# Kernel optimization log

Measured on AMD Instinct MI355X. Metric: run time of the kernel, lower is better.

The kernel has to match this reference:

```python
import jax, jax.numpy as jnp
import numpy as np

B, S, E, H, L, F = 64, 256, 480, 6, 8, 1920
D = E // H  # 80
VOCAB, MEL, CHORD = 4833, 257, 4833 - 257
EPS = 1e-5


def setup_inputs() -> dict:
    key = jax.random.key(0)
    ks = jax.random.split(key, 24)
    mel = jax.random.randint(ks[0], (B, S), 0, MEL)
    chd = MEL + jax.random.randint(ks[1], (B, S), 0, CHORD)
    pos = jnp.arange(S) % 2  # 0=melody, 1=chord
    input_tokens = jnp.where(pos[None, :] == 1, chd, mel)
    std = 0.02
    n = lambda k, shp: std * jax.random.normal(k, shp, dtype=jnp.float32)
    return {
        'input_tokens': input_tokens,
        'tok_emb': n(ks[2], (VOCAB, E)),
        'pos_emb': n(ks[3], (S, E)),
        'Wq': n(ks[4], (L, E, E)), 'bq': jnp.zeros((L, E)),
        'Wk': n(ks[5], (L, E, E)), 'bk': jnp.zeros((L, E)),
        'Wv': n(ks[6], (L, E, E)), 'bv': jnp.zeros((L, E)),
        'Wo': n(ks[7], (L, E, E)), 'bo': jnp.zeros((L, E)),
        'ln1_s': jnp.ones((L, E)), 'ln1_b': jnp.zeros((L, E)),
        'ln2_s': jnp.ones((L, E)), 'ln2_b': jnp.zeros((L, E)),
        'W1': n(ks[8], (L, F, E)), 'b1': jnp.zeros((L, F)),
        'W2': n(ks[9], (L, E, F)), 'b2': jnp.zeros((L, E)),
        'Wh': n(ks[10], (CHORD, E)), 'bh': jnp.zeros((CHORD,)),
    }


def _ln(x, s, b):
    mu = jnp.mean(x, -1, keepdims=True)
    var = jnp.var(x, -1, keepdims=True)
    return (x - mu) * jax.lax.rsqrt(var + EPS) * s + b


def reference(input_tokens, tok_emb, pos_emb, Wq, bq, Wk, bk, Wv, bv, Wo, bo,
              ln1_s, ln1_b, ln2_s, ln2_b, W1, b1, W2, b2, Wh, bh):
    x = tok_emb[input_tokens] + pos_emb[None, :, :]  # [B,S,E]
    causal = jnp.tril(jnp.ones((S, S), dtype=bool))  # True = keep
    scale = 1.0 / jnp.sqrt(jnp.float32(D))
    for i in range(L):
        h = _ln(x, ln1_s[i], ln1_b[i])
        q = (h @ Wq[i].T + bq[i]).reshape(B, S, H, D).transpose(0, 2, 1, 3)
        k = (h @ Wk[i].T + bk[i]).reshape(B, S, H, D).transpose(0, 2, 1, 3)
        v = (h @ Wv[i].T + bv[i]).reshape(B, S, H, D).transpose(0, 2, 1, 3)
        scores = jnp.einsum('bhsd,bhtd->bhst', q, k) * scale
        scores = jnp.where(causal[None, None], scores, -jnp.inf)
        attn = jax.nn.softmax(scores, axis=-1)
        o = jnp.einsum('bhst,bhtd->bhsd', attn, v)
        o = o.transpose(0, 2, 1, 3).reshape(B, S, E)
        x = x + (o @ Wo[i].T + bo[i])
        h2 = _ln(x, ln2_s[i], ln2_b[i])
        ff = jax.nn.gelu(h2 @ W1[i].T + b1[i], approximate=False) @ W2[i].T + b2[i]
        x = x + ff
    chord = x[:, 1::2, :]  # [B, S//2, E]
    return chord @ Wh.T + bh
```

## Files before the change

kernel.cpp:

```cpp
#include <hip/hip_runtime.h>
#include <hip/hip_bf16.h>
#include <math.h>

#define B_ 64
#define S_ 256
#define E_ 480
#define H_ 6
#define D_ 80
#define L_ 8
#define F_ 1920
#define CHORD_ 4576
#define TOKENS_ (B_*S_)
#define CROWS_ (B_*128)
#define QS_ 1440

typedef unsigned short u16;
typedef unsigned int u32;
typedef unsigned long long u64;
typedef __attribute__((ext_vector_type(8))) short short8;
typedef __attribute__((ext_vector_type(4))) float f32x4;
typedef __attribute__((ext_vector_type(4))) u32 u32x4;

__device__ __forceinline__ u16 f2bf(float f){
  u32 u = __float_as_uint(f);
  return (u16)((u + 0x7fffu + ((u >> 16) & 1u)) >> 16);
}

__device__ __forceinline__ void async_cp16(void* lds, const void* g){
  __builtin_amdgcn_global_load_lds((const __attribute__((address_space(1))) void*)g,
                                   (__attribute__((address_space(3))) void*)lds, 16, 0, 0);
}

__device__ __forceinline__ void xcd_tile(int gx, int gy, int& tx, int& ty){
  const int nwg = gx * gy;
  const int bid = blockIdx.y * gx + blockIdx.x;
  const int xcd = bid & 7, slot = bid >> 3;
  const int q8 = nwg >> 3, r8 = nwg & 7;
  const int t = slot + (xcd < r8 ? xcd * (q8 + 1) : r8 * (q8 + 1) + (xcd - r8) * q8);
  ty = t / gx;
  tx = t - ty * gx;
}

__global__ void cvt_kernel(const float* __restrict__ s, u16* __restrict__ d, int n4)
{
  int i = blockIdx.x * 256 + threadIdx.x;
  const int stride = gridDim.x * 256;
  for (; i < n4; i += stride){
    float4 v = ((const float4*)s)[i];
    u64 w = (u64)((u32)f2bf(v.x) | ((u32)f2bf(v.y) << 16))
          | ((u64)((u32)f2bf(v.z) | ((u32)f2bf(v.w) << 16)) << 32);
    ((u64*)d)[i] = w;
  }
}

__global__ void qkv_cvt_kernel(const float* __restrict__ Wq, const float* __restrict__ Wk,
                               const float* __restrict__ Wv, u16* __restrict__ dst)
{
  const int per = E_*E_/4;
  const int tot = L_*3*per;
  int i = blockIdx.x * 256 + threadIdx.x;
  const int stride = gridDim.x * 256;
  for (; i < tot; i += stride){
    int l = i / (3*per);
    int rem = i - l*3*per;
    int sel = rem / per;
    int r2 = rem - sel*per;
    const float* src = (sel == 0) ? Wq : (sel == 1) ? Wk : Wv;
    float4 v = ((const float4*)(src + (size_t)l*E_*E_))[r2];
    u64 w = (u64)((u32)f2bf(v.x) | ((u32)f2bf(v.y) << 16))
          | ((u64)((u32)f2bf(v.z) | ((u32)f2bf(v.w) << 16)) << 32);
    ((u64*)dst)[i] = w;
  }
}

__global__ void bias_cat_kernel(const float* __restrict__ bq, const float* __restrict__ bk,
                                const float* __restrict__ bv, float* __restrict__ dst)
{
  int i = blockIdx.x * 256 + threadIdx.x;
  if (i >= L_*QS_) return;
  int l = i / QS_, c = i - l*QS_;
  float v = (c < 480) ? bq[l*480 + c] : (c < 960) ? bk[l*480 + c - 480] : bv[l*480 + c - 960];
  dst[i] = v;
}

__global__ void embed_kernel(const int* __restrict__ tok,
                             const float* __restrict__ tok_emb,
                             const float* __restrict__ pos_emb,
                             float* __restrict__ x)
{
  int row = blockIdx.x;
  int s = row & (S_-1);
  int t = tok[row];
  const float* te = tok_emb + (size_t)t * E_;
  const float* pe = pos_emb + (size_t)s * E_;
  float* xr = x + (size_t)row * E_;
  for (int e = threadIdx.x; e < E_; e += blockDim.x)
    xr[e] = te[e] + pe[e];
}

__global__ __launch_bounds__(256) void ln_kernel(const float* __restrict__ x,
    const float* __restrict__ g, const float* __restrict__ b, u16* __restrict__ o)
{
  int wid = threadIdx.x >> 6, lane = threadIdx.x & 63;
  int row = blockIdx.x * 4 + wid;
  const float* xr = x + (size_t)row * E_;
  float v[8];
  #pragma unroll
  for (int i = 0; i < 7; ++i) v[i] = xr[lane + i*64];
  v[7] = (lane < 32) ? xr[448 + lane] : 0.f;
  float sum = 0.f, sq = 0.f;
  #pragma unroll
  for (int i = 0; i < 8; ++i){ sum += v[i]; sq += v[i]*v[i]; }
  #pragma unroll
  for (int m = 1; m < 64; m <<= 1){ sum += __shfl_xor(sum, m); sq += __shfl_xor(sq, m); }
  float mean = sum * (1.f/E_);
  float var  = sq  * (1.f/E_) - mean*mean;
  float rs = rsqrtf(var + 1e-5f);
  u16* orow = o + (size_t)row * E_;
  #pragma unroll
  for (int i = 0; i < 7; ++i){
    int idx = lane + i*64;
    orow[idx] = f2bf((v[i]-mean)*rs*g[idx] + b[idx]);
  }
  if (lane < 32){
    int idx = 448 + lane;
    orow[idx] = f2bf((v[7]-mean)*rs*g[idx] + b[idx]);
  }
}

template<int MODE>
__global__ __launch_bounds__(256, 4) void gemm_bf_kernel(const u16* __restrict__ A,
                            const u16* __restrict__ Wb, const float* __restrict__ bias,
                            u16* __restrict__ Cb, float* __restrict__ Cf,
                            int M, int N, int K, int ldc)
{
  __shared__ u16 As[2][128*32];
  __shared__ u16 Ws[2][128*32];
  const int tid = threadIdx.x;
  const int wid = tid >> 6, lane = tid & 63;
  const int wr = wid >> 1, wc = wid & 1;
  const int lr = lane & 15, kg = lane >> 4;
  const int kgs = kg ^ (lr & 3);
  int tx, ty;
  xcd_tile(gridDim.x, gridDim.y, tx, ty);
  const int m0 = ty * 128;
  const int n0 = tx * 128;

  const f32x4 zero = {0.f,0.f,0.f,0.f};
  f32x4 acc[4][4];
  #pragma unroll
  for (int i=0;i<4;i++)
    #pragma unroll
    for (int j=0;j<4;j++)
      acc[i][j] = zero;

  const int srow = tid >> 2;
  const int schunk = (tid & 3) ^ (srow & 3);
  const u16* ap0 = A + (size_t)(m0 + srow) * K + schunk*8;
  const u16* ap1 = ap0 + (size_t)64 * K;
  int r0 = n0 + srow, r1 = r0 + 64;
  if (r0 >= N) r0 = N-1;
  if (r1 >= N) r1 = N-1;
  const u16* wp0 = Wb + (size_t)r0 * K + schunk*8;
  const u16* wp1 = Wb + (size_t)r1 * K + schunk*8;

  #define STAGE(bb, k0) do { \
    char* ab = (char*)As[bb] + wid*1024; \
    char* wb_ = (char*)Ws[bb] + wid*1024; \
    async_cp16(ab,        ap0 + (k0)); \
    async_cp16(ab + 4096, ap1 + (k0)); \
    async_cp16(wb_,        wp0 + (k0)); \
    async_cp16(wb_ + 4096, wp1 + (k0)); \
  } while(0)

  const int nsteps = K >> 5;
  STAGE(0, 0);
  __syncthreads();
  int cur = 0;
  for (int ks = 0; ks < nsteps; ++ks){
    if (ks + 1 < nsteps) STAGE(cur^1, (ks+1) << 5);

    short8 af[4], wf[4];
    #pragma unroll
    for (int i=0;i<4;i++) af[i] = *(const short8*)&As[cur][(wr*64 + i*16 + lr)*32 + kgs*8];
    #pragma unroll
    for (int j=0;j<4;j++) wf[j] = *(const short8*)&Ws[cur][(wc*64 + j*16 + lr)*32 + kgs*8];
    #pragma unroll
    for (int i=0;i<4;i++)
      #pragma unroll
      for (int j=0;j<4;j++)
        acc[i][j] = __builtin_amdgcn_mfma_f32_16x16x32_bf16(af[i], wf[j], acc[i][j], 0, 0, 0);

    __syncthreads();
    cur ^= 1;
  }
  #undef STAGE

  #pragma unroll
  for (int i=0;i<4;i++){
    const int row = m0 + wr*64 + i*16 + kg*4;
    #pragma unroll
    for (int j=0;j<4;j++){
      const int col = n0 + wc*64 + j*16 + lr;
      if (col < N){
        const float bv = bias[col];
        #pragma unroll
        for (int q=0;q<4;q++){
          float val = acc[i][j][q] + bv;
          size_t off = (size_t)(row + q) * ldc + col;
          if (MODE == 0){
            Cb[off] = f2bf(val);
          } else if (MODE == 1){
            float gx = 0.5f * val * (1.f + erff(val * 0.70710678118654752f));
            Cb[off] = f2bf(gx);
          } else if (MODE == 2){
            Cf[off] += val;
          } else {
            Cf[off] = val;
          }
        }
      }
    }
  }
}

template<int MODE>
__global__ __launch_bounds__(256) void gemm_kernel(const u16* __restrict__ A, const float* __restrict__ W,
                            const float* __restrict__ bias,
                            u16* __restrict__ Cb, float* __restrict__ Cf,
                            int M, int N, int K, int ldc)
{
  __shared__ u16 As[128*32];
  __shared__ u16 Ws[128*32];
  const int tid = threadIdx.x;
  const int wid = tid >> 6, lane = tid & 63;
  const int wr = wid >> 1, wc = wid & 1;
  const int lr = lane & 15, kg = lane >> 4;
  int tx, ty;
  xcd_tile(gridDim.x, gridDim.y, tx, ty);
  const int m0 = ty * 128;
  const int n0 = tx * 128;

  const f32x4 zero = {0.f,0.f,0.f,0.f};
  f32x4 acc[4][4];
  #pragma unroll
  for (int i=0;i<4;i++)
    #pragma unroll
    for (int j=0;j<4;j++)
      acc[i][j] = zero;

  const int trow = tid >> 1;
  const int tcol = (tid & 1) * 16;
  const int wn = n0 + trow;
  const bool wok = wn < N;
  const float* wp = W + (size_t)wn * K + tcol;

  const u16* ap0 = A + (size_t)(m0 + (tid>>2)) * K + (tid&3)*8;
  const u16* ap1 = ap0 + (size_t)64 * K;
  char* lb0 = (char*)As + wid*1024;
  char* lb1 = (char*)As + 4096 + wid*1024;
  u32* wdst = (u32*)&Ws[trow*32 + tcol];

  const int nsteps = K >> 5;
  for (int ks = 0; ks < nsteps; ++ks){
    const int k0 = ks << 5;
    async_cp16(lb0, ap0 + k0);
    async_cp16(lb1, ap1 + k0);

    float wv[16];
    if (wok){
      const float4* s4 = (const float4*)(wp + k0);
      #pragma unroll
      for (int i=0;i<4;i++){
        float4 t4 = s4[i];
        wv[4*i]=t4.x; wv[4*i+1]=t4.y; wv[4*i+2]=t4.z; wv[4*i+3]=t4.w;
      }
    } else {
      #pragma unroll
      for (int i=0;i<16;i++) wv[i]=0.f;
    }
    u32 pk[8];
    #pragma unroll
    for (int i=0;i<8;i++) pk[i] = (u32)f2bf(wv[2*i]) | ((u32)f2bf(wv[2*i+1]) << 16);
    #pragma unroll
    for (int i=0;i<8;i++) wdst[i] = pk[i];

    __syncthreads();

    short8 af[4], wf[4];
    #pragma unroll
    for (int i=0;i<4;i++) af[i] = *(const short8*)&As[(wr*64 + i*16 + lr)*32 + kg*8];
    #pragma unroll
    for (int j=0;j<4;j++) wf[j] = *(const short8*)&Ws[(wc*64 + j*16 + lr)*32 + kg*8];
    #pragma unroll
    for (int i=0;i<4;i++)
      #pragma unroll
      for (int j=0;j<4;j++)
        acc[i][j] = __builtin_amdgcn_mfma_f32_16x16x32_bf16(af[i], wf[j], acc[i][j], 0, 0, 0);

    __syncthreads();
  }

  #pragma unroll
  for (int i=0;i<4;i++){
    const int row = m0 + wr*64 + i*16 + kg*4;
    #pragma unroll
    for (int j=0;j<4;j++){
      const int col = n0 + wc*64 + j*16 + lr;
      if (col < N){
        const float bv = bias[col];
        #pragma unroll
        for (int q=0;q<4;q++){
          float val = acc[i][j][q] + bv;
          size_t off = (size_t)(row + q) * ldc + col;
          if (MODE == 0){
            Cb[off] = f2bf(val);
          } else if (MODE == 1){
            float gx = 0.5f * val * (1.f + erff(val * 0.70710678118654752f));
            Cb[off] = f2bf(gx);
          } else if (MODE == 2){
            Cf[off] += val;
          } else {
            Cf[off] = val;
          }
        }
      }
    }
  }
}

#define KSTRIDE 104
#define VSTRIDE 264
__global__ __launch_bounds__(256) void attn_mfma_kernel(const u16* __restrict__ QKV,
                                                        u16* __restrict__ O)
{
  __shared__ u16 ks[256*KSTRIDE];
  __shared__ u16 vt[80*VSTRIDE];
  const int bh = blockIdx.x;
  const int b = bh / H_, h = bh - b*H_;
  const int tid = threadIdx.x;
  const int wv = tid >> 6, lane = tid & 63;
  const int q16 = lane & 15, g = lane >> 4;
  const size_t rowbase = (size_t)(b*S_ + tid) * QS_ + h * D_;

  {
    const uint4* kr = (const uint4*)(QKV + rowbase + 480);
    uint4 t0[10];
    #pragma unroll
    for (int i=0;i<10;i++) t0[i] = kr[i];
    u16* krow = &ks[tid*KSTRIDE];
    #pragma unroll
    for (int i=0;i<10;i++) *(uint4*)&krow[i*8] = t0[i];
    const uint4 z4 = {0,0,0,0};
    *(uint4*)&krow[80] = z4;
    *(uint4*)&krow[88] = z4;
  }
  {
    const u32* vr = (const u32*)(QKV + rowbase + 960);
    u32 t1[40];
    #pragma unroll
    for (int i=0;i<40;i++) t1[i] = vr[i];
    #pragma unroll
    for (int i=0;i<40;i++){
      vt[(2*i)*VSTRIDE + tid]   = (u16)(t1[i] & 0xffffu);
      vt[(2*i+1)*VSTRIDE + tid] = (u16)(t1[i] >> 16);
    }
  }
  short8 bq[4][3];
  const short8 z8 = {0,0,0,0,0,0,0,0};
  #pragma unroll
  for (int i=0;i<4;i++){
    const int qr = 16*wv + 64*i;
    const u16* qrow = QKV + (size_t)(b*S_ + qr + q16) * QS_ + h*D_;
    bq[i][0] = *(const short8*)&qrow[g*8];
    bq[i][1] = *(const short8*)&qrow[32 + g*8];
    bq[i][2] = (g < 2) ? *(const short8*)&qrow[64 + g*8] : z8;
  }
  __syncthreads();

  f32x4 o_[4][5];
  float m_[4], l_[4];
  #pragma unroll
  for (int i=0;i<4;i++){
    m_[i] = -1e30f; l_[i] = 0.f;
    #pragma unroll
    for (int j=0;j<5;j++) o_[i][j] = (f32x4){0.f,0.f,0.f,0.f};
  }
  const float scale = 0.1118033988749895f;
  const int ktmaxw = (16*wv + 207) >> 5;

  for (int kt = 0; kt <= ktmaxw; ++kt){
    short8 af[2][3];
    #pragma unroll
    for (int a=0;a<2;a++)
      #pragma unroll
      for (int kk=0;kk<3;kk++)
        af[a][kk] = *(const short8*)&ks[(32*kt + 16*a + q16)*KSTRIDE + kk*32 + g*8];
    short8 bvv[5];
    #pragma unroll
    for (int j=0;j<5;j++)
      bvv[j] = *(const short8*)&vt[(16*j + q16)*VSTRIDE + kt*32 + g*8];

    #pragma unroll
    for (int i=0;i<4;i++){
      const int qr = 16*wv + 64*i;
      if (kt > ((qr + 15) >> 5)) continue;
      f32x4 c0 = {0.f,0.f,0.f,0.f}, c1 = {0.f,0.f,0.f,0.f};
      #pragma unroll
      for (int kk=0;kk<3;kk++){
        c0 = __builtin_amdgcn_mfma_f32_16x16x32_bf16(af[0][kk], bq[i][kk], c0, 0, 0, 0);
        c1 = __builtin_amdgcn_mfma_f32_16x16x32_bf16(af[1][kk], bq[i][kk], c1, 0, 0, 0);
      }
      const int qglob = qr + q16;
      const int kb0 = 32*kt + 4*g;
      const bool diag = (32*kt + 31) > qr;
      float s0[4], s1[4];
      #pragma unroll
      for (int r=0;r<4;r++){
        s0[r] = c0[r] * scale;
        s1[r] = c1[r] * scale;
        if (diag){
          if (kb0 + r > qglob)      s0[r] = -3e38f;
          if (kb0 + 16 + r > qglob) s1[r] = -3e38f;
        }
      }
      float mx = fmaxf(fmaxf(fmaxf(s0[0],s0[1]),fmaxf(s0[2],s0[3])),
                       fmaxf(fmaxf(s1[0],s1[1]),fmaxf(s1[2],s1[3])));
      mx = fmaxf(mx, __shfl_xor(mx, 16));
      mx = fmaxf(mx, __shfl_xor(mx, 32));
      const float mnew = fmaxf(m_[i], mx);
      const float resc = __expf(m_[i] - mnew);
      float p0[4], p1[4], ps = 0.f;
      #pragma unroll
      for (int r=0;r<4;r++){
        p0[r] = __expf(s0[r] - mnew);
        p1[r] = __expf(s1[r] - mnew);
        ps += p0[r] + p1[r];
      }
      ps += __shfl_xor(ps, 16);
      ps += __shfl_xor(ps, 32);
      l_[i] = l_[i] * resc + ps;
      m_[i] = mnew;
      float fr[4];
      #pragma unroll
      for (int r=0;r<4;r++) fr[r] = __shfl(resc, 4*g + r);
      #pragma unroll
      for (int j=0;j<5;j++){
        #pragma unroll
        for (int r=0;r<4;r++) o_[i][j][r] *= fr[r];
      }
      u32 pw0 = (u32)f2bf(p0[0]) | ((u32)f2bf(p0[1]) << 16);
      u32 pw1 = (u32)f2bf(p0[2]) | ((u32)f2bf(p0[3]) << 16);
      u32 pw2 = (u32)f2bf(p1[0]) | ((u32)f2bf(p1[1]) << 16);
      u32 pw3 = (u32)f2bf(p1[2]) | ((u32)f2bf(p1[3]) << 16);
      const int s01 = ((((g<<1)&3)<<4) + q16) << 2;
      const int s23 = (((((g<<1)+1)&3)<<4) + q16) << 2;
      int rA0 = __builtin_amdgcn_ds_bpermute(s01, (int)pw0);
      int rB0 = __builtin_amdgcn_ds_bpermute(s01, (int)pw2);
      int rA1 = __builtin_amdgcn_ds_bpermute(s01, (int)pw1);
      int rB1 = __builtin_amdgcn_ds_bpermute(s01, (int)pw3);
      int rA2 = __builtin_amdgcn_ds_bpermute(s23, (int)pw0);
      int rB2 = __builtin_amdgcn_ds_bpermute(s23, (int)pw2);
      int rA3 = __builtin_amdgcn_ds_bpermute(s23, (int)pw1);
      int rB3 = __builtin_amdgcn_ds_bpermute(s23, (int)pw3);
      const bool lo = (g < 2);
      u32x4 rw = { (u32)(lo ? rA0 : rB0), (u32)(lo ? rA1 : rB1),
                   (u32)(lo ? rA2 : rB2), (u32)(lo ? rA3 : rB3) };
      short8 pa = __builtin_bit_cast(short8, rw);
      #pragma unroll
      for (int j=0;j<5;j++)
        o_[i][j] = __builtin_amdgcn_mfma_f32_16x16x32_bf16(pa, bvv[j], o_[i][j], 0, 0, 0);
    }
  }

  #pragma unroll
  for (int i=0;i<4;i++){
    const int qr = 16*wv + 64*i;
    const float inv = 1.f / l_[i];
    float fr[4];
    #pragma unroll
    for (int r=0;r<4;r++) fr[r] = __shfl(inv, 4*g + r);
    #pragma unroll
    for (int j=0;j<5;j++){
      #pragma unroll
      for (int r=0;r<4;r++){
        const int row = qr + 4*g + r;
        O[(size_t)(b*S_ + row) * E_ + h*D_ + 16*j + q16] = f2bf(o_[i][j][r] * fr[r]);
      }
    }
  }
}

__global__ void gather_kernel(const float* __restrict__ x, u16* __restrict__ cin)
{
  int i = blockIdx.x * 256 + threadIdx.x;
  if (i >= CROWS_*E_) return;
  int row = i / E_, col = i - row*E_;
  int b = row >> 7, r = row & 127;
  cin[i] = f2bf(x[((size_t)(b*S_ + 2*r + 1))*E_ + col]);
}

extern "C" void kernel_launch(void* const* d_in, const int* in_sizes, int n_in,
                              void* d_out, int out_size, void* d_ws, size_t ws_size,
                              hipStream_t stream)
{
  (void)in_sizes; (void)n_in; (void)out_size;
  const int*   tok     = (const int*)d_in[0];
  const float* tok_emb = (const float*)d_in[1];
  const float* pos_emb = (const float*)d_in[2];
  const float* Wq = (const float*)d_in[3];
  const float* bq = (const float*)d_in[4];
  const float* Wk = (const float*)d_in[5];
  const float* bk = (const float*)d_in[6];
  const float* Wv = (const float*)d_in[7];
  const float* bv = (const float*)d_in[8];
  const float* Wo = (const float*)d_in[9];
  const float* bo = (const float*)d_in[10];
  const float* ln1s = (const float*)d_in[11];
  const float* ln1b = (const float*)d_in[12];
  const float* ln2s = (const float*)d_in[13];
  const float* ln2b = (const float*)d_in[14];
  const float* W1 = (const float*)d_in[15];
  const float* b1 = (const float*)d_in[16];
  const float* W2 = (const float*)d_in[17];
  const float* b2 = (const float*)d_in[18];
  const float* Wh = (const float*)d_in[19];
  const float* bh = (const float*)d_in[20];

  char* p = (char*)d_ws;
  float* x  = (float*)p;            p += (size_t)TOKENS_*E_*4;
  u16* h    = (u16*)p;              p += (size_t)TOKENS_*E_*2;
  u16* qkv  = (u16*)p;
  u16* ao   = qkv + (size_t)TOKENS_*QS_;
  u16* ff1  = qkv;
  u16* cin  = h;
  p += (size_t)TOKENS_*QS_*2 + (size_t)TOKENS_*E_*2;

  const size_t szE  = (size_t)L_*E_*E_;
  const size_t szF  = (size_t)L_*F_*E_;
  const size_t szH  = (size_t)CHORD_*E_;
  u16* wqkv_bf = (u16*)p;            p += 3*szE*2;
  u16* wo_bf   = (u16*)p;            p += szE*2;
  u16* w1_bf   = (u16*)p;            p += szF*2;
  u16* w2_bf   = (u16*)p;            p += szF*2;
  u16* wh_bf   = (u16*)p;            p += szH*2;
  float* bqkv  = (float*)p;          p += (size_t)L_*QS_*4;
  const size_t need = (size_t)(p - (char*)d_ws);
  const bool bf16w = (ws_size >= need);

  embed_kernel<<<TOKENS_, 128, 0, stream>>>(tok, tok_emb, pos_emb, x);

  dim3 blk(256);
  dim3 gQKV(12, TOKENS_/128);
  dim3 gE(4, TOKENS_/128);
  dim3 gF1(15, TOKENS_/128);
  dim3 gHd(36, CROWS_/128);

  if (bf16w){
    qkv_cvt_kernel<<<2048, blk, 0, stream>>>(Wq, Wk, Wv, wqkv_bf);
    bias_cat_kernel<<<(L_*QS_ + 255)/256, blk, 0, stream>>>(bq, bk, bv, bqkv);
    cvt_kernel<<<1024, blk, 0, stream>>>(Wo, wo_bf, (int)(szE/4));
    cvt_kernel<<<1024, blk, 0, stream>>>(W1, w1_bf, (int)(szF/4));
    cvt_kernel<<<1024, blk, 0, stream>>>(W2, w2_bf, (int)(szF/4));
    cvt_kernel<<<1024, blk, 0, stream>>>(Wh, wh_bf, (int)(szH/4));
    for (int i = 0; i < L_; ++i){
      ln_kernel<<<TOKENS_/4, blk, 0, stream>>>(x, ln1s + i*E_, ln1b + i*E_, h);
      gemm_bf_kernel<0><<<gQKV, blk, 0, stream>>>(h, wqkv_bf + (size_t)i*3*E_*E_, bqkv + i*QS_, qkv, nullptr, TOKENS_, QS_, E_, QS_);
      attn_mfma_kernel<<<B_*H_, blk, 0, stream>>>(qkv, ao);
      gemm_bf_kernel<2><<<gE, blk, 0, stream>>>(ao, wo_bf + (size_t)i*E_*E_, bo + i*E_, nullptr, x, TOKENS_, E_, E_, E_);
      ln_kernel<<<TOKENS_/4, blk, 0, stream>>>(x, ln2s + i*E_, ln2b + i*E_, h);
      gemm_bf_kernel<1><<<gF1, blk, 0, stream>>>(h, w1_bf + (size_t)i*F_*E_, b1 + i*F_, ff1, nullptr, TOKENS_, F_, E_, F_);
      gemm_bf_kernel<2><<<gE, blk, 0, stream>>>(ff1, w2_bf + (size_t)i*E_*F_, b2 + i*E_, nullptr, x, TOKENS_, E_, F_, E_);
    }
    gather_kernel<<<(CROWS_*E_ + 255)/256, blk, 0, stream>>>(x, cin);
    gemm_bf_kernel<3><<<gHd, blk, 0, stream>>>(cin, wh_bf, bh, nullptr, (float*)d_out, CROWS_, CHORD_, E_, CHORD_);
  } else {
    for (int i = 0; i < L_; ++i){
      ln_kernel<<<TOKENS_/4, blk, 0, stream>>>(x, ln1s + i*E_, ln1b + i*E_, h);
      gemm_kernel<0><<<gE, blk, 0, stream>>>(h, Wq + (size_t)i*E_*E_, bq + i*E_, qkv, nullptr, TOKENS_, E_, E_, QS_);
      gemm_kernel<0><<<gE, blk, 0, stream>>>(h, Wk + (size_t)i*E_*E_, bk + i*E_, qkv + 480, nullptr, TOKENS_, E_, E_, QS_);
      gemm_kernel<0><<<gE, blk, 0, stream>>>(h, Wv + (size_t)i*E_*E_, bv + i*E_, qkv + 960, nullptr, TOKENS_, E_, E_, QS_);
      attn_mfma_kernel<<<B_*H_, blk, 0, stream>>>(qkv, ao);
      gemm_kernel<2><<<gE, blk, 0, stream>>>(ao, Wo + (size_t)i*E_*E_, bo + i*E_, nullptr, x, TOKENS_, E_, E_, E_);
      ln_kernel<<<TOKENS_/4, blk, 0, stream>>>(x, ln2s + i*E_, ln2b + i*E_, h);
      gemm_kernel<1><<<gF1, blk, 0, stream>>>(h, W1 + (size_t)i*F_*E_, b1 + i*F_, ff1, nullptr, TOKENS_, F_, E_, F_);
      gemm_kernel<2><<<gE, blk, 0, stream>>>(ff1, W2 + (size_t)i*E_*F_, b2 + i*E_, nullptr, x, TOKENS_, E_, F_, E_);
    }
    gather_kernel<<<(CROWS_*E_ + 255)/256, blk, 0, stream>>>(x, cin);
    gemm_kernel<3><<<gHd, blk, 0, stream>>>(cin, Wh, bh, nullptr, (float*)d_out, CROWS_, CHORD_, E_, CHORD_);
  }
}
```

Baseline: 2.147 ms.

## Add 256x128-tile GEMM and pad the K dimension to 512 for tall GEMMs

Adds a 512-thread GEMM kernel with 256x128 output tiles, used for the QKV, FFN1, FFN2 and head projections. The goal is more operand reuse per LDS stage and fewer blocks per GEMM. To give K=480 operands a clean multiple of the tile, the layernorm output, the gathered head input and the QKV, W1 and Wh bf16 weights are stored zero-padded to a stride of 512. This adds roughly 7% redundant MFMA work and extra memory traffic on those GEMMs. The larger tiles also raise register and LDS pressure, which can lower occupancy.

Result: no change. 2.155 ms (+0.3%).

```diff
diff --git a/kernel.cpp b/kernel.cpp
--- a/kernel.cpp
+++ b/kernel.cpp
@@ -13,6 +13,7 @@
 #define TOKENS_ (B_*S_)
 #define CROWS_ (B_*128)
 #define QS_ 1440
+#define KP_ 512
 
 typedef unsigned short u16;
 typedef unsigned int u32;
@@ -53,22 +54,42 @@
   }
 }
 
-__global__ void qkv_cvt_kernel(const float* __restrict__ Wq, const float* __restrict__ Wk,
-                               const float* __restrict__ Wv, u16* __restrict__ dst)
-{
-  const int per = E_*E_/4;
-  const int tot = L_*3*per;
+__global__ void cvt_pad_kernel(const float* __restrict__ s, u16* __restrict__ d, int nrows)
+{
+  const int tot = nrows * 128;
   int i = blockIdx.x * 256 + threadIdx.x;
   const int stride = gridDim.x * 256;
   for (; i < tot; i += stride){
-    int l = i / (3*per);
-    int rem = i - l*3*per;
-    int sel = rem / per;
-    int r2 = rem - sel*per;
-    const float* src = (sel == 0) ? Wq : (sel == 1) ? Wk : Wv;
-    float4 v = ((const float4*)(src + (size_t)l*E_*E_))[r2];
-    u64 w = (u64)((u32)f2bf(v.x) | ((u32)f2bf(v.y) << 16))
-          | ((u64)((u32)f2bf(v.z) | ((u32)f2bf(v.w) << 16)) << 32);
+    int row = i >> 7, c4 = i & 127;
+    u64 w = 0;
+    if (c4 < 120){
+      float4 v = ((const float4*)(s + (size_t)row * E_))[c4];
+      w = (u64)((u32)f2bf(v.x) | ((u32)f2bf(v.y) << 16))
+        | ((u64)((u32)f2bf(v.z) | ((u32)f2bf(v.w) << 16)) << 32);
+    }
+    ((u64*)d)[i] = w;
+  }
+}
+
+__global__ void qkv_cvt_kernel(const float* __restrict__ Wq, const float* __restrict__ Wk,
+                               const float* __restrict__ Wv, u16* __restrict__ dst)
+{
+  const int tot = L_ * QS_ * 128;
+  int i = blockIdx.x * 256 + threadIdx.x;
+  const int stride = gridDim.x * 256;
+  for (; i < tot; i += stride){
+    int l = i / (QS_*128);
+    int rem = i - l*(QS_*128);
+    int row = rem >> 7, c4 = rem & 127;
+    u64 w = 0;
+    if (c4 < 120){
+      const float* src = (row < 480) ? Wq + (size_t)l*E_*E_ + (size_t)row*E_
+                       : (row < 960) ? Wk + (size_t)l*E_*E_ + (size_t)(row-480)*E_
+                                     : Wv + (size_t)l*E_*E_ + (size_t)(row-960)*E_;
+      float4 v = ((const float4*)src)[c4];
+      w = (u64)((u32)f2bf(v.x) | ((u32)f2bf(v.y) << 16))
+        | ((u64)((u32)f2bf(v.z) | ((u32)f2bf(v.w) << 16)) << 32);
+    }
     ((u64*)dst)[i] = w;
   }
 }
@@ -99,7 +120,8 @@
 }
 
 __global__ __launch_bounds__(256) void ln_kernel(const float* __restrict__ x,
-    const float* __restrict__ g, const float* __restrict__ b, u16* __restrict__ o)
+    const float* __restrict__ g, const float* __restrict__ b, u16* __restrict__ o,
+    int ldo, int pad)
 {
   int wid = threadIdx.x >> 6, lane = threadIdx.x & 63;
   int row = blockIdx.x * 4 + wid;
@@ -116,7 +138,7 @@
   float mean = sum * (1.f/E_);
   float var  = sq  * (1.f/E_) - mean*mean;
   float rs = rsqrtf(var + 1e-5f);
-  u16* orow = o + (size_t)row * E_;
+  u16* orow = o + (size_t)row * ldo;
   #pragma unroll
   for (int i = 0; i < 7; ++i){
     int idx = lane + i*64;
@@ -125,6 +147,100 @@
   if (lane < 32){
     int idx = 448 + lane;
     orow[idx] = f2bf((v[7]-mean)*rs*g[idx] + b[idx]);
+  }
+  if (pad && lane < 32) orow[480 + lane] = 0;
+}
+
+template<int MODE>
+__global__ __launch_bounds__(512) void gemm_tall_kernel(const u16* __restrict__ A,
+                            const u16* __restrict__ Wb, const float* __restrict__ bias,
+                            u16* __restrict__ Cb, float* __restrict__ Cf,
+                            int M, int N, int K, int ldc)
+{
+  __shared__ u16 As[2][256*32];
+  __shared__ u16 Ws[2][128*32];
+  const int tid = threadIdx.x;
+  const int wid = tid >> 6, lane = tid & 63;
+  const int wm = wid >> 1, wn = wid & 1;
+  const int lr = lane & 15, kg = lane >> 4;
+  const int kgs = kg ^ (lr & 3);
+  int tx, ty;
+  xcd_tile(gridDim.x, gridDim.y, tx, ty);
+  const int m0 = ty * 256;
+  const int n0 = tx * 128;
+
+  const f32x4 zero = {0.f,0.f,0.f,0.f};
+  f32x4 acc[4][4];
+  #pragma unroll
+  for (int i=0;i<4;i++)
+    #pragma unroll
+    for (int j=0;j<4;j++)
+      acc[i][j] = zero;
+
+  const int srow = tid >> 2;
+  const int schunk = (tid & 3) ^ (srow & 3);
+  const u16* ap0 = A + (size_t)(m0 + srow) * K + schunk*8;
+  const u16* ap1 = ap0 + (size_t)128 * K;
+  int r0 = n0 + srow;
+  if (r0 >= N) r0 = N-1;
+  const u16* wp0 = Wb + (size_t)r0 * K + schunk*8;
+
+  #define STAGE(bb, k0) do { \
+    char* ab = (char*)As[bb] + wid*1024; \
+    char* wb_ = (char*)Ws[bb] + wid*1024; \
+    async_cp16(ab,        ap0 + (k0)); \
+    async_cp16(ab + 8192, ap1 + (k0)); \
+    async_cp16(wb_,        wp0 + (k0)); \
+  } while(0)
+
+  const int nsteps = K >> 5;
+  STAGE(0, 0);
+  __syncthreads();
+  int cur = 0;
+  for (int ks = 0; ks < nsteps; ++ks){
+    if (ks + 1 < nsteps) STAGE(cur^1, (ks+1) << 5);
+
+    short8 af[4], wf[4];
+    #pragma unroll
+    for (int i=0;i<4;i++) af[i] = *(const short8*)&As[cur][(wm*64 + i*16 + lr)*32 + kgs*8];
+    #pragma unroll
+    for (int j=0;j<4;j++) wf[j] = *(const short8*)&Ws[cur][(wn*64 + j*16 + lr)*32 + kgs*8];
+    #pragma unroll
+    for (int i=0;i<4;i++)
+      #pragma unroll
+      for (int j=0;j<4;j++)
+        acc[i][j] = __builtin_amdgcn_mfma_f32_16x16x32_bf16(af[i], wf[j], acc[i][j], 0, 0, 0);
+
+    __syncthreads();
+    cur ^= 1;
+  }
+  #undef STAGE
+
+  #pragma unroll
+  for (int i=0;i<4;i++){
+    const int row = m0 + wm*64 + i*16 + kg*4;
+    #pragma unroll
+    for (int j=0;j<4;j++){
+      const int col = n0 + wn*64 + j*16 + lr;
+      if (col < N){
+        const float bv = bias[col];
+        #pragma unroll
+        for (int q=0;q<4;q++){
+          float val = acc[i][j][q] + bv;
+          size_t off = (size_t)(row + q) * ldc + col;
+          if (MODE == 0){
+            Cb[off] = f2bf(val);
+          } else if (MODE == 1){
+            float gx = 0.5f * val * (1.f + erff(val * 0.70710678118654752f));
+            Cb[off] = f2bf(gx);
+          } else if (MODE == 2){
+            Cf[off] += val;
+          } else {
+            Cf[off] = val;
+          }
+        }
+      }
+    }
   }
 }
 
@@ -491,13 +607,13 @@
   }
 }
 
-__global__ void gather_kernel(const float* __restrict__ x, u16* __restrict__ cin)
+__global__ void gather_kernel(const float* __restrict__ x, u16* __restrict__ cin, int ld)
 {
   int i = blockIdx.x * 256 + threadIdx.x;
-  if (i >= CROWS_*E_) return;
-  int row = i / E_, col = i - row*E_;
+  if (i >= CROWS_*ld) return;
+  int row = i / ld, col = i - row*ld;
   int b = row >> 7, r = row & 127;
-  cin[i] = f2bf(x[((size_t)(b*S_ + 2*r + 1))*E_ + col]);
+  cin[i] = (col < E_) ? f2bf(x[((size_t)(b*S_ + 2*r + 1))*E_ + col]) : (u16)0;
 }
 
 extern "C" void kernel_launch(void* const* d_in, const int* in_sizes, int n_in,
@@ -529,7 +645,7 @@
 
   char* p = (char*)d_ws;
   float* x  = (float*)p;            p += (size_t)TOKENS_*E_*4;
-  u16* h    = (u16*)p;              p += (size_t)TOKENS_*E_*2;
+  u16* h    = (u16*)p;              p += (size_t)TOKENS_*KP_*2;
   u16* qkv  = (u16*)p;
   u16* ao   = qkv + (size_t)TOKENS_*QS_;
   u16* ff1  = qkv;
@@ -537,13 +653,11 @@
   p += (size_t)TOKENS_*QS_*2 + (size_t)TOKENS_*E_*2;
 
   const size_t szE  = (size_t)L_*E_*E_;
-  const size_t szF  = (size_t)L_*F_*E_;
-  const size_t szH  = (size_t)CHORD_*E_;
-  u16* wqkv_bf = (u16*)p;            p += 3*szE*2;
+  u16* wqkv_bf = (u16*)p;            p += (size_t)L_*QS_*KP_*2;
   u16* wo_bf   = (u16*)p;            p += szE*2;
-  u16* w1_bf   = (u16*)p;            p += szF*2;
-  u16* w2_bf   = (u16*)p;            p += szF*2;
-  u16* wh_bf   = (u16*)p;            p += szH*2;
+  u16* w1_bf   = (u16*)p;            p += (size_t)L_*F_*KP_*2;
+  u16* w2_bf   = (u16*)p;            p += (size_t)L_*E_*F_*2;
+  u16* wh_bf   = (u16*)p;            p += (size_t)CHORD_*KP_*2;
   float* bqkv  = (float*)p;          p += (size_t)L_*QS_*4;
   const size_t need = (size_t)(p - (char*)d_ws);
   const bool bf16w = (ws_size >= need);
@@ -551,42 +665,39 @@
   embed_kernel<<<TOKENS_, 128, 0, stream>>>(tok, tok_emb, pos_emb, x);
 
   dim3 blk(256);
-  dim3 gQKV(12, TOKENS_/128);
-  dim3 gE(4, TOKENS_/128);
-  dim3 gF1(15, TOKENS_/128);
-  dim3 gHd(36, CROWS_/128);
+  dim3 blk512(512);
 
   if (bf16w){
     qkv_cvt_kernel<<<2048, blk, 0, stream>>>(Wq, Wk, Wv, wqkv_bf);
     bias_cat_kernel<<<(L_*QS_ + 255)/256, blk, 0, stream>>>(bq, bk, bv, bqkv);
     cvt_kernel<<<1024, blk, 0, stream>>>(Wo, wo_bf, (int)(szE/4));
-    cvt_kernel<<<1024, blk, 0, stream>>>(W1, w1_bf, (int)(szF/4));
-    cvt_kernel<<<1024, blk, 0, stream>>>(W2, w2_bf, (int)(szF/4));
-    cvt_kernel<<<1024, blk, 0, stream>>>(Wh, wh_bf, (int)(szH/4));
+    cvt_pad_kernel<<<2048, blk, 0, stream>>>(W1, w1_bf, L_*F_);
+    cvt_kernel<<<1024, blk, 0, stream>>>(W2, w2_bf, (int)((size_t)L_*E_*F_/4));
+    cvt_pad_kernel<<<1024, blk, 0, stream>>>(Wh, wh_bf, CHORD_);
     for (int i = 0; i < L_; ++i){
-      ln_kernel<<<TOKENS_/4, blk, 0, stream>>>(x, ln1s + i*E_, ln1b + i*E_, h);
-      gemm_bf_kernel<0><<<gQKV, blk, 0, stream>>>(h, wqkv_bf + (size_t)i*3*E_*E_, bqkv + i*QS_, qkv, nullptr, TOKENS_, QS_, E_, QS_);
+      ln_kernel<<<TOKENS_/4, blk, 0, stream>>>(x, ln1s + i*E_, ln1b + i*E_, h, KP_, 1);
+      gemm_tall_kernel<0><<<dim3(12, 64), blk512, 0, stream>>>(h, wqkv_bf + (size_t)i*QS_*KP_, bqkv + i*QS_, qkv, nullptr, TOKENS_, QS_, KP_, QS_);
       attn_mfma_kernel<<<B_*H_, blk, 0, stream>>>(qkv, ao);
-      gemm_bf_kernel<2><<<gE, blk, 0, stream>>>(ao, wo_bf + (size_t)i*E_*E_, bo + i*E_, nullptr, x, TOKENS_, E_, E_, E_);
-      ln_kernel<<<TOKENS_/4, blk, 0, stream>>>(x, ln2s + i*E_, ln2b + i*E_, h);
-      gemm_bf_kernel<1><<<gF1, blk, 0, stream>>>(h, w1_bf + (size_t)i*F_*E_, b1 + i*F_, ff1, nullptr, TOKENS_, F_, E_, F_);
-      gemm_bf_kernel<2><<<gE, blk, 0, stream>>>(ff1, w2_bf + (size_t)i*E_*F_, b2 + i*E_, nullptr, x, TOKENS_, E_, F_, E_);
-    }
-    gather_kernel<<<(CROWS_*E_ + 255)/256, blk, 0, stream>>>(x, cin);
-    gemm_bf_kernel<3><<<gHd, blk, 0, stream>>>(cin, wh_bf, bh, nullptr, (float*)d_out, CROWS_, CHORD_, E_, CHORD_);
+      gemm_bf_kernel<2><<<dim3(4, 128), blk, 0, stream>>>(ao, wo_bf + (size_t)i*E_*E_, bo + i*E_, nullptr, x, TOKENS_, E_, E_, E_);
+      ln_kernel<<<TOKENS_/4, blk, 0, stream>>>(x, ln2s + i*E_, ln2b + i*E_, h, KP_, 1);
+      gemm_tall_kernel<1><<<dim3(15, 64), blk512, 0, stream>>>(h, w1_bf + (size_t)i*F_*KP_, b1 + i*F_, ff1, nullptr, TOKENS_, F_, KP_, F_);
+      gemm_tall_kernel<2><<<dim3(4, 64), blk512, 0, stream>>>(ff1, w2_bf + (size_t)i*E_*F_, b2 + i*E_, nullptr, x, TOKENS_, E_, F_, E_);
+    }
+    gather_kernel<<<(CROWS_*KP_ + 255)/256, blk, 0, stream>>>(x, cin, KP_);
+    gemm_tall_kernel<3><<<dim3(36, 32), blk512, 0, stream>>>(cin, wh_bf, bh, nullptr, (float*)d_out, CROWS_, CHORD_, KP_, CHORD_);
   } else {
     for (int i = 0; i < L_; ++i){
-      ln_kernel<<<TOKENS_/4, blk, 0, stream>>>(x, ln1s + i*E_, ln1b + i*E_, h);
-      gemm_kernel<0><<<gE, blk, 0, stream>>>(h, Wq + (size_t)i*E_*E_, bq + i*E_, qkv, nullptr, TOKENS_, E_, E_, QS_);
-      gemm_kernel<0><<<gE, blk, 0, stream>>>(h, Wk + (size_t)i*E_*E_, bk + i*E_, qkv + 480, nullptr, TOKENS_, E_, E_, QS_);
-      gemm_kernel<0><<<gE, blk, 0, stream>>>(h, Wv + (size_t)i*E_*E_, bv + i*E_, qkv + 960, nullptr, TOKENS_, E_, E_, QS_);
+      ln_kernel<<<TOKENS_/4, blk, 0, stream>>>(x, ln1s + i*E_, ln1b + i*E_, h, E_, 0);
+      gemm_kernel<0><<<dim3(4, 128), blk, 0, stream>>>(h, Wq + (size_t)i*E_*E_, bq + i*E_, qkv, nullptr, TOKENS_, E_, E_, QS_);
+      gemm_kernel<0><<<dim3(4, 128), blk, 0, stream>>>(h, Wk + (size_t)i*E_*E_, bk + i*E_, qkv + 480, nullptr, TOKENS_, E_, E_, QS_);
+      gemm_kernel<0><<<dim3(4, 128), blk, 0, stream>>>(h, Wv + (size_t)i*E_*E_, bv + i*E_, qkv + 960, nullptr, TOKENS_, E_, E_, QS_);
       attn_mfma_kernel<<<B_*H_, blk, 0, stream>>>(qkv, ao);
-      gemm_kernel<2><<<gE, blk, 0, stream>>>(ao, Wo + (size_t)i*E_*E_, bo + i*E_, nullptr, x, TOKENS_, E_, E_, E_);
-      ln_kernel<<<TOKENS_/4, blk, 0, stream>>>(x, ln2s + i*E_, ln2b + i*E_, h);
-      gemm_kernel<1><<<gF1, blk, 0, stream>>>(h, W1 + (size_t)i*F_*E_, b1 + i*F_, ff1, nullptr, TOKENS_, F_, E_, F_);
-      gemm_kernel<2><<<gE, blk, 0, stream>>>(ff1, W2 + (size_t)i*E_*F_, b2 + i*E_, nullptr, x, TOKENS_, E_, F_, E_);
-    }
-    gather_kernel<<<(CROWS_*E_ + 255)/256, blk, 0, stream>>>(x, cin);
-    gemm_kernel<3><<<gHd, blk, 0, stream>>>(cin, Wh, bh, nullptr, (float*)d_out, CROWS_, CHORD_, E_, CHORD_);
-  }
-}
+      gemm_kernel<2><<<dim3(4, 128), blk, 0, stream>>>(ao, Wo + (size_t)i*E_*E_, bo + i*E_, nullptr, x, TOKENS_, E_, E_, E_);
+      ln_kernel<<<TOKENS_/4, blk, 0, stream>>>(x, ln2s + i*E_, ln2b + i*E_, h, E_, 0);
+      gemm_kernel<1><<<dim3(15, 128), blk, 0, stream>>>(h, W1 + (size_t)i*F_*E_, b1 + i*F_, ff1, nullptr, TOKENS_, F_, E_, F_);
+      gemm_kernel<2><<<dim3(4, 128), blk, 0, stream>>>(ff1, W2 + (size_t)i*E_*F_, b2 + i*E_, nullptr, x, TOKENS_, E_, F_, E_);
+    }
+    gather_kernel<<<(CROWS_*E_ + 255)/256, blk, 0, stream>>>(x, cin, E_);
+    gemm_kernel<3><<<dim3(36, 64), blk, 0, stream>>>(cin, Wh, bh, nullptr, (float*)d_out, CROWS_, CHORD_, E_, CHORD_);
+  }
+}
```
